# Kernel optimization log

Measured on AMD Instinct MI355X. Metric: run time of the kernel, lower is better.

Reference implementation:

```python
import jax, jax.numpy as jnp
import numpy as np
from jax import lax

NPOINT = 1024
NSAMPLE = 32
RADIUS = 0.6
BN_EPS = 1e-5


def square_distance(src, dst):
    # src (B,S,3), dst (B,N,3) -> (B,S,N) squared distances
    d = -2.0 * jnp.einsum('bsc,bnc->bsn', src, dst)
    d = d + jnp.sum(src ** 2, -1)[:, :, None]
    d = d + jnp.sum(dst ** 2, -1)[:, None, :]
    return d


def farthest_point_sample(xyz, npoint):
    B, N, _ = xyz.shape
    bidx = jnp.arange(B)

    def step(carry, _):
        distance, farthest = carry
        centroid = xyz[bidx, farthest]                      # (B,3)
        dist = jnp.sum((xyz - centroid[:, None, :]) ** 2, -1)  # (B,N)
        distance = jnp.minimum(distance, dist)
        new_far = jnp.argmax(distance, -1)
        return (distance, new_far), farthest

    init = (jnp.full((B, N), 1e10, xyz.dtype), jnp.zeros((B,), jnp.int32))
    _, idxs = lax.scan(step, init, None, length=npoint)
    return idxs.T                                            # (B,npoint)


def ball_query(xyz, new_xyz, radius, nsample):
    B, N, _ = xyz.shape
    sqr = square_distance(new_xyz, xyz)                      # (B,S,N)
    idx = jnp.where(sqr <= radius ** 2, jnp.arange(N)[None, None, :], N)
    idx = jnp.sort(idx, axis=-1)[:, :, :nsample]             # (B,S,K)
    first = idx[:, :, :1]
    return jnp.where(idx == N, first, idx)


def gather2(points, idx):
    # points (B,N,C), idx (B,S) -> (B,S,C)
    return jax.vmap(lambda p, i: p[i])(points, idx)


def gather3(points, idx):
    # points (B,N,C), idx (B,S,K) -> (B,S,K,C)
    return jax.vmap(lambda p, i: p[i])(points, idx)


def sa_forward(xyz, features, params):
    fps_idx = lax.stop_gradient(farthest_point_sample(xyz, NPOINT))
    new_xyz = gather2(xyz, fps_idx)                          # (B,S,3)
    idx = lax.stop_gradient(ball_query(xyz, new_xyz, RADIUS, NSAMPLE))
    grouped_xyz = gather3(xyz, idx) - new_xyz[:, :, None, :] # (B,S,K,3)
    grouped_feat = gather3(features.transpose(0, 2, 1), idx) # (B,S,K,C)
    g = jnp.concatenate([grouped_xyz, grouped_feat], -1)     # (B,S,K,C+3)
    g = g.transpose(0, 3, 2, 1)                              # (B,Cin,K,S)
    for w, b, ga, be in params:
        g = jnp.einsum('oc,bcks->boks', w, g) + b[None, :, None, None]
        mu = jnp.mean(g, axis=(0, 2, 3), keepdims=True)
        var = jnp.var(g, axis=(0, 2, 3), keepdims=True)
        g = ga[None, :, None, None] * (g - mu) * lax.rsqrt(var + BN_EPS) \
            + be[None, :, None, None]
        g = jax.nn.relu(g)
    new_features = jnp.max(g, axis=2)                        # (B,Cout,S)
    return new_xyz, new_features


def setup_inputs() -> dict:
    key = jax.random.key(0)
    ks = jax.random.split(key, 8)
    B, N, C = 16, 4096, 128
    cin = C + 3
    mlp = [128, 128, 256]
    inp = {
        'xyz': jax.random.normal(ks[0], (B, N, 3), jnp.float32),
        'features': jax.random.normal(ks[1], (B, C, N), jnp.float32),
    }
    prev = cin
    for i, out in enumerate(mlp):
        inp[f'w{i}'] = jax.random.normal(ks[2 + i], (out, prev), jnp.float32) * 0.05
        inp[f'b{i}'] = jnp.zeros((out,), jnp.float32)
        inp[f'gamma{i}'] = jnp.ones((out,), jnp.float32)
        inp[f'beta{i}'] = jnp.zeros((out,), jnp.float32)
        prev = out
    return inp


def reference(xyz, features, w0, b0, gamma0, beta0, w1, b1, gamma1, beta1,
              w2, b2, gamma2, beta2):
    params = [(w0, b0, gamma0, beta0), (w1, b1, gamma1, beta1),
              (w2, b2, gamma2, beta2)]
    return sa_forward(xyz, features, params)
```

## Files before the change

### kernel.cpp

```cpp
#include <hip/hip_runtime.h>

#define B_ 16
#define N_ 4096
#define S_ 1024
#define K_ 32
#define PITCH2 136
#define PITCH1 168

typedef unsigned long long u64;
typedef short bf16x8 __attribute__((ext_vector_type(8)));
typedef unsigned short u16x8 __attribute__((ext_vector_type(8)));
typedef float f32x4 __attribute__((ext_vector_type(4)));
typedef float f32x2 __attribute__((ext_vector_type(2)));

__device__ __forceinline__ unsigned short f2bf(float f) {
  unsigned u = __float_as_uint(f);
  unsigned r = (u + 0x7FFFu + ((u >> 16) & 1u)) >> 16;
  return (unsigned short)r;
}
__device__ __forceinline__ float bf2f(unsigned short h) {
  return __uint_as_float(((unsigned)h) << 16);
}

#define DPP_MAX(v, ctrl)                                                        \
  {                                                                             \
    int _t = __builtin_amdgcn_update_dpp(__float_as_int(v), __float_as_int(v),  \
                                         ctrl, 0xf, 0xf, false);                \
    v = fmaxf(v, __int_as_float(_t));                                           \
  }

__global__ __launch_bounds__(512) void k_front(
    const float* __restrict__ xyz, float* __restrict__ new_xyz,
    const float* __restrict__ feat, unsigned short* __restrict__ featT,
    const float* __restrict__ w0, const float* __restrict__ w1,
    const float* __restrict__ w2, unsigned short* __restrict__ wbf0,
    unsigned short* __restrict__ wbf1, unsigned short* __restrict__ wbf2,
    float* __restrict__ stats) {
  __shared__ __align__(16) float smem[N_ * 4 + S_ + 64];
  int blk = blockIdx.x, t = threadIdx.x;

  if (blk < 16) {
#pragma clang fp contract(off)
#if __has_builtin(__builtin_amdgcn_s_setprio)
    __builtin_amdgcn_s_setprio(3);
#endif
    float4* pts = (float4*)smem;
    int* idxs = (int*)(smem + N_ * 4);
    u64* swk = (u64*)(smem + N_ * 4 + S_);
    int b = blk;
    const float* base = xyz + (size_t)b * N_ * 3;
    for (int i = t; i < N_; i += 512)
      pts[i] = make_float4(base[i * 3], base[i * 3 + 1], base[i * 3 + 2], 0.0f);
    if (t == 0) idxs[0] = 0;
    __syncthreads();
    f32x2 px[4], py[4], pz[4], pd[4];
    int i0 = t * 8;
    #pragma unroll
    for (int j = 0; j < 4; ++j) {
      float4 p0 = pts[i0 + 2 * j], p1 = pts[i0 + 2 * j + 1];
      px[j] = (f32x2){p0.x, p1.x};
      py[j] = (f32x2){p0.y, p1.y};
      pz[j] = (f32x2){p0.z, p1.z};
      pd[j] = (f32x2){1e10f, 1e10f};
    }
    int cur = 0;
    for (int it = 0; it < S_; ++it) {
      float4 c = pts[cur];
      f32x2 c2x = (f32x2){c.x, c.x}, c2y = (f32x2){c.y, c.y}, c2z = (f32x2){c.z, c.z};
      float bestv = -1.0f; int besti = 0;
      #pragma unroll
      for (int j = 0; j < 4; ++j) {
        f32x2 dx = px[j] - c2x;
        f32x2 dy = py[j] - c2y;
        f32x2 dz = pz[j] - c2z;
        f32x2 d = (dx * dx + dy * dy) + dz * dz;
        f32x2 dm = __builtin_elementwise_min(pd[j], d);
        pd[j] = dm;
        if (dm.x > bestv) { bestv = dm.x; besti = 2 * j; }
        if (dm.y > bestv) { bestv = dm.y; besti = 2 * j + 1; }
      }
      float v = bestv;
      DPP_MAX(v, 0x111);
      DPP_MAX(v, 0x112);
      DPP_MAX(v, 0x114);
      DPP_MAX(v, 0x118);
      DPP_MAX(v, 0x142);
      DPP_MAX(v, 0x143);
      float wmax = __int_as_float(__builtin_amdgcn_readlane(__float_as_int(v), 63));
      u64 mask = __ballot(bestv == wmax);
      int owner = __ffsll((long long)mask) - 1;
      int widx = __builtin_amdgcn_readlane(i0 + besti, owner);
      if ((t & 63) == 0)
        swk[(it & 1) * 8 + (t >> 6)] =
            ((u64)__float_as_uint(wmax) << 32) | (unsigned)(4095 - widx);
      __syncthreads();
      const u64* kk = swk + (it & 1) * 8;
      u64 k0 = kk[0];
      #pragma unroll
      for (int w = 1; w < 8; ++w) if (kk[w] > k0) k0 = kk[w];
      cur = 4095 - (int)(unsigned)(k0 & 0xFFFFFFFFull);
      if (t == 0 && it + 1 < S_) idxs[it + 1] = cur;
    }
    __syncthreads();
    for (int i = t; i < S_; i += 512) {
      float4 v = pts[idxs[i]];
      size_t o = ((size_t)b * S_ + i) * 3;
      new_xyz[o] = v.x; new_xyz[o + 1] = v.y; new_xyz[o + 2] = v.z;
    }
  } else if (blk < 32) {
    int id = (blk - 16) * 512 + t;
    const int st = 16 * 512;
    for (int i = id; i < 32768; i += st) stats[i] = 0.0f;
    for (int i = id; i < 128 * 160; i += st) {
      int n = i / 160, k = i - n * 160;
      float v = (k < 128) ? w0[n * 131 + 3 + k] : (k < 131) ? w0[n * 131 + k - 128] : 0.0f;
      wbf0[i] = f2bf(v);
    }
    for (int i = id; i < 128 * 128; i += st) wbf1[i] = f2bf(w1[i]);
    for (int i = id; i < 256 * 128; i += st) wbf2[i] = f2bf(w2[i]);
  } else {
    float (*tile)[33] = (float(*)[33])smem;
    int blk2 = blk - 32;
    int n0 = (blk2 & 127) * 32;
    int c0 = ((blk2 >> 7) & 3) * 32;
    int b = blk2 >> 9;
    int tx = t & 31, ty = t >> 5;
    #pragma unroll
    for (int j = 0; j < 32; j += 16)
      tile[ty + j][tx] = feat[((size_t)b * 128 + c0 + ty + j) * N_ + n0 + tx];
    __syncthreads();
    #pragma unroll
    for (int j = 0; j < 32; j += 16)
      featT[((size_t)b * N_ + n0 + ty + j) * 128 + c0 + tx] = f2bf(tile[tx][ty + j]);
  }
}

__global__ __launch_bounds__(256) void k_ballq(const float* __restrict__ xyz,
                                               const float* __restrict__ new_xyz,
                                               int* __restrict__ ball_idx) {
  int b = blockIdx.y;
  int s = blockIdx.x * 4 + (threadIdx.x >> 6);
  int lane = threadIdx.x & 63;
  const float* pb = xyz + (size_t)b * N_ * 3;
  size_t q = (size_t)b * S_ + s;
  float qx = new_xyz[q * 3], qy = new_xyz[q * 3 + 1], qz = new_xyz[q * 3 + 2];
  float sq = __fadd_rn(__fadd_rn(__fmul_rn(qx, qx), __fmul_rn(qy, qy)), __fmul_rn(qz, qz));
  int* out = ball_idx + q * K_;
  int total = 0;
  int first_idx = -1;
  for (int basei = 0; basei < N_; basei += 64) {
    int i = basei + lane;
    float fx = pb[i * 3], fy = pb[i * 3 + 1], fz = pb[i * 3 + 2];
    float dot = __fmul_rn(qx, fx);
    dot = __fadd_rn(dot, __fmul_rn(qy, fy));
    dot = __fadd_rn(dot, __fmul_rn(qz, fz));
    float sd = __fadd_rn(__fadd_rn(__fmul_rn(fx, fx), __fmul_rn(fy, fy)), __fmul_rn(fz, fz));
    float dist = __fadd_rn(__fadd_rn(__fmul_rn(-2.0f, dot), sq), sd);
    bool within = (dist <= 0.36f);
    u64 m = __ballot(within);
    if (first_idx < 0 && m) first_idx = basei + __ffsll((long long)m) - 1;
    if (within) {
      int pos = total + __popcll(m & ((1ull << lane) - 1ull));
      if (pos < K_) out[pos] = i;
    }
    total += (int)__popcll(m);
    if (total >= K_) break;
  }
  if (total < K_) {
    int k2 = total + lane;
    if (k2 < K_) out[k2] = first_idx;
  }
}

#define MFMA(a, b, c) __builtin_amdgcn_mfma_f32_16x16x32_bf16(a, b, c, 0, 0, 0)
#define NTILES 4096

__global__ __launch_bounds__(256) void k_layer1(
    const float* __restrict__ xyz, const float* __restrict__ new_xyz,
    const unsigned short* __restrict__ featT, const int* __restrict__ ball_idx,
    const unsigned short* __restrict__ wbf0, const float* __restrict__ b0,
    unsigned short* __restrict__ y, float* __restrict__ stats) {
  __shared__ __align__(16) unsigned short Wl[128 * PITCH1];
  __shared__ float sbias[128];
  int t = threadIdx.x;
  int w = t >> 6, L = t & 63, lm = L & 15, lg = L >> 4;
  {
    int n = t >> 1, h = t & 1;
    const uint4* wr = (const uint4*)(wbf0 + n * 160 + h * 80);
    uint4* wl = (uint4*)(Wl + n * PITCH1 + h * 80);
    #pragma unroll
    for (int i = 0; i < 10; ++i) wl[i] = wr[i];
    if (t < 128) sbias[t] = b0[t];
  }
  __syncthreads();

  for (int tile = blockIdx.x; tile < NTILES; tile += gridDim.x) {
    int bb = tile >> 8;
    int s0 = (tile & 255) * 4;
    size_t qg = (size_t)bb * S_ + s0 + w;

    int p0 = ball_idx[qg * K_ + lm];
    int p1 = ball_idx[qg * K_ + 16 + lm];
    const unsigned short* f0 = featT + ((size_t)bb * N_ + p0) * 128;
    const unsigned short* f1 = featT + ((size_t)bb * N_ + p1) * 128;
    bf16x8 a0[5], a1[5];
    #pragma unroll
    for (int kt = 0; kt < 4; ++kt) {
      a0[kt] = *(const bf16x8*)(f0 + kt * 32 + lg * 8);
      a1[kt] = *(const bf16x8*)(f1 + kt * 32 + lg * 8);
    }
    a0[4] = (bf16x8){0, 0, 0, 0, 0, 0, 0, 0};
    a1[4] = (bf16x8){0, 0, 0, 0, 0, 0, 0, 0};
    if (lg == 0) {
      float nx = new_xyz[qg * 3], ny = new_xyz[qg * 3 + 1], nz = new_xyz[qg * 3 + 2];
      const float* pp0 = xyz + ((size_t)bb * N_ + p0) * 3;
      const float* pp1 = xyz + ((size_t)bb * N_ + p1) * 3;
      a0[4][0] = (short)f2bf(pp0[0] - nx);
      a0[4][1] = (short)f2bf(pp0[1] - ny);
      a0[4][2] = (short)f2bf(pp0[2] - nz);
      a1[4][0] = (short)f2bf(pp1[0] - nx);
      a1[4][1] = (short)f2bf(pp1[1] - ny);
      a1[4][2] = (short)f2bf(pp1[2] - nz);
    }
    f32x4 acc[2][8];
    #pragma unroll
    for (int mi = 0; mi < 2; ++mi)
      #pragma unroll
      for (int nt = 0; nt < 8; ++nt) acc[mi][nt] = (f32x4){0.f, 0.f, 0.f, 0.f};
    #pragma unroll
    for (int kt = 0; kt < 5; ++kt) {
      int ko = kt * 32 + lg * 8;
      bf16x8 bv[8];
      #pragma unroll
      for (int nt = 0; nt < 8; ++nt)
        bv[nt] = *(const bf16x8*)&Wl[(nt * 16 + lm) * PITCH1 + ko];
      #pragma unroll
      for (int nt = 0; nt < 8; ++nt) {
        acc[0][nt] = MFMA(a0[kt], bv[nt], acc[0][nt]);
        acc[1][nt] = MFMA(a1[kt], bv[nt], acc[1][nt]);
      }
    }
    int slot = tile & 31;
    #pragma unroll
    for (int nt = 0; nt < 8; ++nt) {
      int col = nt * 16 + lm;
      float bo = sbias[col];
      float s1 = 0.f, s2 = 0.f;
      #pragma unroll
      for (int mi = 0; mi < 2; ++mi)
        #pragma unroll
        for (int r = 0; r < 4; ++r) {
          float yv = acc[mi][nt][r] + bo;
          s1 += yv; s2 += yv * yv;
          int ks = mi * 16 + lg * 4 + r;
          y[(qg * K_ + ks) * 128 + col] = f2bf(yv);
        }
      s1 += __shfl_xor(s1, 16); s2 += __shfl_xor(s2, 16);
      s1 += __shfl_xor(s1, 32); s2 += __shfl_xor(s2, 32);
      if (lg == 0) {
        atomicAdd(stats + ((size_t)slot * 128 + col) * 2, s1);
        atomicAdd(stats + ((size_t)slot * 128 + col) * 2 + 1, s2);
      }
    }
  }
}

__global__ __launch_bounds__(256) void k_layer2(
    unsigned short* y, const float* __restrict__ stats,
    const float* __restrict__ gamma, const float* __restrict__ beta,
    const unsigned short* __restrict__ wbf1, const float* __restrict__ b1,
    float* __restrict__ stats2) {
  __shared__ __align__(16) unsigned short Wl[128 * PITCH2];
  __shared__ __align__(16) float sa[128], sd[128];
  __shared__ float sbias[128];
  int t = threadIdx.x;
  int w = t >> 6, L = t & 63, lm = L & 15, lg = L >> 4;
  if (t < 128) {
    float s1 = 0.0f, s2 = 0.0f;
    for (int sl = 0; sl < 32; ++sl) {
      s1 += stats[((size_t)sl * 128 + t) * 2];
      s2 += stats[((size_t)sl * 128 + t) * 2 + 1];
    }
    const float inv = 1.0f / 524288.0f;
    float mu = s1 * inv;
    float var = s2 * inv - mu * mu;
    float a = gamma[t] * rsqrtf(var + 1e-5f);
    sa[t] = a;
    sd[t] = beta[t] - a * mu;
    sbias[t] = b1[t];
  }
  {
    int n = t >> 1, h = t & 1;
    const uint4* wr = (const uint4*)(wbf1 + n * 128 + h * 64);
    uint4* wl = (uint4*)(Wl + n * PITCH2 + h * 64);
    #pragma unroll
    for (int i = 0; i < 8; ++i) wl[i] = wr[i];
  }
  __syncthreads();

  for (int tile = blockIdx.x; tile < NTILES; tile += gridDim.x) {
    int bb = tile >> 8;
    int s0 = (tile & 255) * 4;
    size_t qg = (size_t)bb * S_ + s0 + w;

    const u16x8* yr0 = (const u16x8*)(y + (qg * K_ + lm) * 128);
    const u16x8* yr1 = (const u16x8*)(y + (qg * K_ + 16 + lm) * 128);
    u16x8 raw0[4], raw1[4];
    #pragma unroll
    for (int kt = 0; kt < 4; ++kt) { raw0[kt] = yr0[kt * 4 + lg]; raw1[kt] = yr1[kt * 4 + lg]; }
    bf16x8 a0[4], a1[4];
    #pragma unroll
    for (int kt = 0; kt < 4; ++kt) {
      int c = kt * 32 + lg * 8;
      f32x4 A0 = *(const f32x4*)&sa[c], A1 = *(const f32x4*)&sa[c + 4];
      f32x4 D0 = *(const f32x4*)&sd[c], D1 = *(const f32x4*)&sd[c + 4];
      #pragma unroll
      for (int j = 0; j < 4; ++j) {
        a0[kt][j]     = (short)f2bf(fmaxf(A0[j] * bf2f(raw0[kt][j])     + D0[j], 0.f));
        a0[kt][j + 4] = (short)f2bf(fmaxf(A1[j] * bf2f(raw0[kt][j + 4]) + D1[j], 0.f));
        a1[kt][j]     = (short)f2bf(fmaxf(A0[j] * bf2f(raw1[kt][j])     + D0[j], 0.f));
        a1[kt][j + 4] = (short)f2bf(fmaxf(A1[j] * bf2f(raw1[kt][j + 4]) + D1[j], 0.f));
      }
    }
    f32x4 acc[2][8];
    #pragma unroll
    for (int mi = 0; mi < 2; ++mi)
      #pragma unroll
      for (int nt = 0; nt < 8; ++nt) acc[mi][nt] = (f32x4){0.f, 0.f, 0.f, 0.f};
    #pragma unroll
    for (int kt = 0; kt < 4; ++kt) {
      int ko = kt * 32 + lg * 8;
      bf16x8 bv[8];
      #pragma unroll
      for (int nt = 0; nt < 8; ++nt)
        bv[nt] = *(const bf16x8*)&Wl[(nt * 16 + lm) * PITCH2 + ko];
      #pragma unroll
      for (int nt = 0; nt < 8; ++nt) {
        acc[0][nt] = MFMA(a0[kt], bv[nt], acc[0][nt]);
        acc[1][nt] = MFMA(a1[kt], bv[nt], acc[1][nt]);
      }
    }
    int slot = tile & 31;
    #pragma unroll
    for (int nt = 0; nt < 8; ++nt) {
      int col = nt * 16 + lm;
      float bo = sbias[col];
      float s1 = 0.f, s2 = 0.f;
      #pragma unroll
      for (int mi = 0; mi < 2; ++mi)
        #pragma unroll
        for (int r = 0; r < 4; ++r) {
          float yv = acc[mi][nt][r] + bo;
          s1 += yv; s2 += yv * yv;
          int ks = mi * 16 + lg * 4 + r;
          y[(qg * K_ + ks) * 128 + col] = f2bf(yv);
        }
      s1 += __shfl_xor(s1, 16); s2 += __shfl_xor(s2, 16);
      s1 += __shfl_xor(s1, 32); s2 += __shfl_xor(s2, 32);
      if (lg == 0) {
        atomicAdd(stats2 + ((size_t)slot * 128 + col) * 2, s1);
        atomicAdd(stats2 + ((size_t)slot * 128 + col) * 2 + 1, s2);
      }
    }
  }
}

__global__ __launch_bounds__(256) void k_layer3(
    const unsigned short* __restrict__ y, const float* __restrict__ stats2,
    const float* __restrict__ gamma, const float* __restrict__ beta,
    const unsigned short* __restrict__ wbf2, const float* __restrict__ b2,
    unsigned short* __restrict__ ymax, unsigned short* __restrict__ ymin,
    float* __restrict__ stats3) {
  __shared__ __align__(16) unsigned short Wl[128 * PITCH2];
  __shared__ __align__(16) float sa[128], sd[128];
  __shared__ float sbias[128];
  int nh = blockIdx.y, t = threadIdx.x;
  int w = t >> 6, L = t & 63, lm = L & 15, lg = L >> 4;
  if (t < 128) {
    float s1 = 0.0f, s2 = 0.0f;
    for (int sl = 0; sl < 32; ++sl) {
      s1 += stats2[((size_t)sl * 128 + t) * 2];
      s2 += stats2[((size_t)sl * 128 + t) * 2 + 1];
    }
    const float inv = 1.0f / 524288.0f;
    float mu = s1 * inv;
    float var = s2 * inv - mu * mu;
    float a = gamma[t] * rsqrtf(var + 1e-5f);
    sa[t] = a;
    sd[t] = beta[t] - a * mu;
    sbias[t] = b2[nh * 128 + t];
  }
  {
    int n = t >> 1, h = t & 1;
    const uint4* wr = (const uint4*)(wbf2 + (size_t)(nh * 128 + n) * 128 + h * 64);
    uint4* wl = (uint4*)(Wl + n * PITCH2 + h * 64);
    #pragma unroll
    for (int i = 0; i < 8; ++i) wl[i] = wr[i];
  }
  __syncthreads();

  for (int tile = blockIdx.x; tile < NTILES; tile += gridDim.x) {
    int bb = tile >> 8;
    int s0 = (tile & 255) * 4;
    size_t qg = (size_t)bb * S_ + s0 + w;

    const u16x8* yr0 = (const u16x8*)(y + (qg * K_ + lm) * 128);
    const u16x8* yr1 = (const u16x8*)(y + (qg * K_ + 16 + lm) * 128);
    u16x8 raw0[4], raw1[4];
    #pragma unroll
    for (int kt = 0; kt < 4; ++kt) { raw0[kt] = yr0[kt * 4 + lg]; raw1[kt] = yr1[kt * 4 + lg]; }
    bf16x8 a0[4], a1[4];
    #pragma unroll
    for (int kt = 0; kt < 4; ++kt) {
      int c = kt * 32 + lg * 8;
      f32x4 A0 = *(const f32x4*)&sa[c], A1 = *(const f32x4*)&sa[c + 4];
      f32x4 D0 = *(const f32x4*)&sd[c], D1 = *(const f32x4*)&sd[c + 4];
      #pragma unroll
      for (int j = 0; j < 4; ++j) {
        a0[kt][j]     = (short)f2bf(fmaxf(A0[j] * bf2f(raw0[kt][j])     + D0[j], 0.f));
        a0[kt][j + 4] = (short)f2bf(fmaxf(A1[j] * bf2f(raw0[kt][j + 4]) + D1[j], 0.f));
        a1[kt][j]     = (short)f2bf(fmaxf(A0[j] * bf2f(raw1[kt][j])     + D0[j], 0.f));
        a1[kt][j + 4] = (short)f2bf(fmaxf(A1[j] * bf2f(raw1[kt][j + 4]) + D1[j], 0.f));
      }
    }
    f32x4 acc[2][8];
    #pragma unroll
    for (int mi = 0; mi < 2; ++mi)
      #pragma unroll
      for (int nt = 0; nt < 8; ++nt) acc[mi][nt] = (f32x4){0.f, 0.f, 0.f, 0.f};
    #pragma unroll
    for (int kt = 0; kt < 4; ++kt) {
      int ko = kt * 32 + lg * 8;
      bf16x8 bv[8];
      #pragma unroll
      for (int nt = 0; nt < 8; ++nt)
        bv[nt] = *(const bf16x8*)&Wl[(nt * 16 + lm) * PITCH2 + ko];
      #pragma unroll
      for (int nt = 0; nt < 8; ++nt) {
        acc[0][nt] = MFMA(a0[kt], bv[nt], acc[0][nt]);
        acc[1][nt] = MFMA(a1[kt], bv[nt], acc[1][nt]);
      }
    }
    int slot = tile & 31;
    #pragma unroll
    for (int nt = 0; nt < 8; ++nt) {
      int col = nt * 16 + lm;
      int o = nh * 128 + col;
      float bo = sbias[col];
      float s1 = 0.f, s2 = 0.f, mx = -3.4e38f, mn = 3.4e38f;
      #pragma unroll
      for (int mi = 0; mi < 2; ++mi)
        #pragma unroll
        for (int r = 0; r < 4; ++r) {
          float yv = acc[mi][nt][r] + bo;
          s1 += yv; s2 += yv * yv;
          mx = fmaxf(mx, yv); mn = fminf(mn, yv);
        }
      s1 += __shfl_xor(s1, 16); s2 += __shfl_xor(s2, 16);
      s1 += __shfl_xor(s1, 32); s2 += __shfl_xor(s2, 32);
      mx = fmaxf(mx, __shfl_xor(mx, 16)); mx = fmaxf(mx, __shfl_xor(mx, 32));
      mn = fminf(mn, __shfl_xor(mn, 16)); mn = fminf(mn, __shfl_xor(mn, 32));
      if (lg == 0) {
        ymax[qg * 256 + o] = f2bf(mx);
        ymin[qg * 256 + o] = f2bf(mn);
        atomicAdd(stats3 + ((size_t)slot * 256 + o) * 2, s1);
        atomicAdd(stats3 + ((size_t)slot * 256 + o) * 2 + 1, s2);
      }
    }
  }
}

__global__ __launch_bounds__(256) void k_final(const unsigned short* __restrict__ ymax,
                                               const unsigned short* __restrict__ ymin,
                                               const float* __restrict__ stats3,
                                               const float* __restrict__ gamma,
                                               const float* __restrict__ beta,
                                               float* __restrict__ out2) {
  __shared__ float tile[32][33];
  __shared__ float smA[32], smD[32];
  int b = blockIdx.z, o0 = blockIdx.y * 32, s0 = blockIdx.x * 32;
  int tx = threadIdx.x, ty = threadIdx.y;
  if (ty == 0) {
    int c = o0 + tx;
    float s1 = 0.0f, s2 = 0.0f;
    for (int sl = 0; sl < 32; ++sl) {
      s1 += stats3[((size_t)sl * 256 + c) * 2];
      s2 += stats3[((size_t)sl * 256 + c) * 2 + 1];
    }
    const float inv = 1.0f / 524288.0f;
    float mu = s1 * inv;
    float var = s2 * inv - mu * mu;
    float a = gamma[c] * rsqrtf(var + 1e-5f);
    smA[tx] = a;
    smD[tx] = beta[c] - a * mu;
  }
  __syncthreads();
  float a_rd = smA[tx];
  #pragma unroll
  for (int j = 0; j < 32; j += 8) {
    size_t src = ((size_t)b * S_ + s0 + ty + j) * 256 + o0 + tx;
    tile[ty + j][tx] = (a_rd >= 0.0f) ? bf2f(ymax[src]) : bf2f(ymin[src]);
  }
  __syncthreads();
  #pragma unroll
  for (int j = 0; j < 32; j += 8) {
    float a = smA[ty + j], dd = smD[ty + j];
    out2[((size_t)b * 256 + o0 + ty + j) * S_ + s0 + tx] = fmaxf(a * tile[tx][ty + j] + dd, 0.0f);
  }
}

extern "C" void kernel_launch(void* const* d_in, const int* in_sizes, int n_in,
                              void* d_out, int out_size, void* d_ws, size_t ws_size,
                              hipStream_t stream) {
  (void)in_sizes; (void)n_in; (void)out_size; (void)ws_size;
  const float* xyz  = (const float*)d_in[0];
  const float* feat = (const float*)d_in[1];
  const float* w0   = (const float*)d_in[2];
  const float* b0   = (const float*)d_in[3];
  const float* ga0  = (const float*)d_in[4];
  const float* be0  = (const float*)d_in[5];
  const float* w1   = (const float*)d_in[6];
  const float* b1   = (const float*)d_in[7];
  const float* ga1  = (const float*)d_in[8];
  const float* be1  = (const float*)d_in[9];
  const float* w2   = (const float*)d_in[10];
  const float* b2   = (const float*)d_in[11];
  const float* ga2  = (const float*)d_in[12];
  const float* be2  = (const float*)d_in[13];

  float* out_xyz  = (float*)d_out;
  float* out_feat = out_xyz + (size_t)B_ * S_ * 3;

  char* ws = (char*)d_ws;
  size_t off = 0;
  auto alloc = [&](size_t bytes) -> void* {
    void* p = ws + off;
    off += (bytes + 255) & ~(size_t)255;
    return p;
  };
  unsigned short* featT = (unsigned short*)alloc((size_t)B_ * N_ * 128 * 2);
  int*   ball  = (int*)alloc((size_t)B_ * S_ * K_ * 4);
  float* stats = (float*)alloc(32768 * 4);
  unsigned short* wbf0 = (unsigned short*)alloc(128 * 160 * 2);
  unsigned short* wbf1 = (unsigned short*)alloc(128 * 128 * 2);
  unsigned short* wbf2 = (unsigned short*)alloc(256 * 128 * 2);
  unsigned short* ymaxb = (unsigned short*)alloc((size_t)B_ * S_ * 256 * 2);
  unsigned short* yminb = (unsigned short*)alloc((size_t)B_ * S_ * 256 * 2);
  unsigned short* y = (unsigned short*)alloc((size_t)B_ * S_ * K_ * 128 * 2);

  k_front<<<16 + 16 + 8192, 512, 0, stream>>>(xyz, out_xyz, feat, featT,
                                              w0, w1, w2, wbf0, wbf1, wbf2, stats);
  k_ballq<<<dim3(256, 16), 256, 0, stream>>>(xyz, out_xyz, ball);
  k_layer1<<<768, 256, 0, stream>>>(xyz, out_xyz, featT, ball, wbf0, b0, y, stats);
  k_layer2<<<1024, 256, 0, stream>>>(y, stats, ga0, be0, wbf1, b1, stats + 8192);
  k_layer3<<<dim3(512, 2), 256, 0, stream>>>(y, stats + 8192, ga1, be1, wbf2, b2,
                                             ymaxb, yminb, stats + 16384);
  k_final<<<dim3(32, 8, 16), dim3(32, 8), 0, stream>>>(ymaxb, yminb, stats + 16384,
                                                       ga2, be2, out_feat);
}
```

Before: 1.084 ms.

## Run farthest point sampling in a single wavefront to remove block barriers

The FPS loop now runs in a single 64-lane wavefront per batch. Each lane keeps 64 points in registers, so the per-iteration __syncthreads and the shared-memory cross-wave argmax are gone. The argmax becomes a DPP max reduction followed by a DPP min over matching indices, which picks the lowest index on ties. The block size drops to 256 with launch bounds (256,1), and the transpose and weight-conversion branches are adjusted to match. The cost is heavy register pressure (128 float2 arrays) and a serial chain run by one wave, with the other three waves of the block idle.

```diff
diff --git a/kernel.cpp b/kernel.cpp
--- a/kernel.cpp
+++ b/kernel.cpp
@@ -22,14 +22,19 @@
   return __uint_as_float(((unsigned)h) << 16);
 }
 
-#define DPP_MAX(v, ctrl)                                                        \
+#define DPP_MAXF(v, ctrl)                                                       \
   {                                                                             \
     int _t = __builtin_amdgcn_update_dpp(__float_as_int(v), __float_as_int(v),  \
                                          ctrl, 0xf, 0xf, false);                \
     v = fmaxf(v, __int_as_float(_t));                                           \
   }
-
-__global__ __launch_bounds__(512) void k_front(
+#define DPP_MINI(v, ctrl)                                                       \
+  {                                                                             \
+    int _t = __builtin_amdgcn_update_dpp(v, v, ctrl, 0xf, 0xf, false);          \
+    v = min(v, _t);                                                             \
+  }
+
+__global__ __launch_bounds__(256, 1) void k_front(
     const float* __restrict__ xyz, float* __restrict__ new_xyz,
     const float* __restrict__ feat, unsigned short* __restrict__ featT,
     const float* __restrict__ w0, const float* __restrict__ w1,
@@ -46,70 +51,86 @@
 #endif
     float4* pts = (float4*)smem;
     int* idxs = (int*)(smem + N_ * 4);
-    u64* swk = (u64*)(smem + N_ * 4 + S_);
     int b = blk;
     const float* base = xyz + (size_t)b * N_ * 3;
-    for (int i = t; i < N_; i += 512)
+    for (int i = t; i < N_; i += 256)
       pts[i] = make_float4(base[i * 3], base[i * 3 + 1], base[i * 3 + 2], 0.0f);
     if (t == 0) idxs[0] = 0;
     __syncthreads();
-    f32x2 px[4], py[4], pz[4], pd[4];
-    int i0 = t * 8;
-    #pragma unroll
-    for (int j = 0; j < 4; ++j) {
-      float4 p0 = pts[i0 + 2 * j], p1 = pts[i0 + 2 * j + 1];
-      px[j] = (f32x2){p0.x, p1.x};
-      py[j] = (f32x2){p0.y, p1.y};
-      pz[j] = (f32x2){p0.z, p1.z};
-      pd[j] = (f32x2){1e10f, 1e10f};
-    }
-    int cur = 0;
-    for (int it = 0; it < S_; ++it) {
-      float4 c = pts[cur];
-      f32x2 c2x = (f32x2){c.x, c.x}, c2y = (f32x2){c.y, c.y}, c2z = (f32x2){c.z, c.z};
-      float bestv = -1.0f; int besti = 0;
-      #pragma unroll
-      for (int j = 0; j < 4; ++j) {
-        f32x2 dx = px[j] - c2x;
-        f32x2 dy = py[j] - c2y;
-        f32x2 dz = pz[j] - c2z;
-        f32x2 d = (dx * dx + dy * dy) + dz * dz;
-        f32x2 dm = __builtin_elementwise_min(pd[j], d);
-        pd[j] = dm;
-        if (dm.x > bestv) { bestv = dm.x; besti = 2 * j; }
-        if (dm.y > bestv) { bestv = dm.y; besti = 2 * j + 1; }
-      }
-      float v = bestv;
-      DPP_MAX(v, 0x111);
-      DPP_MAX(v, 0x112);
-      DPP_MAX(v, 0x114);
-      DPP_MAX(v, 0x118);
-      DPP_MAX(v, 0x142);
-      DPP_MAX(v, 0x143);
-      float wmax = __int_as_float(__builtin_amdgcn_readlane(__float_as_int(v), 63));
-      u64 mask = __ballot(bestv == wmax);
-      int owner = __ffsll((long long)mask) - 1;
-      int widx = __builtin_amdgcn_readlane(i0 + besti, owner);
-      if ((t & 63) == 0)
-        swk[(it & 1) * 8 + (t >> 6)] =
-            ((u64)__float_as_uint(wmax) << 32) | (unsigned)(4095 - widx);
-      __syncthreads();
-      const u64* kk = swk + (it & 1) * 8;
-      u64 k0 = kk[0];
-      #pragma unroll
-      for (int w = 1; w < 8; ++w) if (kk[w] > k0) k0 = kk[w];
-      cur = 4095 - (int)(unsigned)(k0 & 0xFFFFFFFFull);
-      if (t == 0 && it + 1 < S_) idxs[it + 1] = cur;
+
+    if (t < 64) {
+      int L = t;
+      f32x2 px[32], py[32], pz[32], pd[32];
+      #pragma unroll
+      for (int j = 0; j < 32; ++j) {
+        float4 p = pts[(2 * j) * 64 + L];
+        float4 q = pts[(2 * j + 1) * 64 + L];
+        px[j] = (f32x2){p.x, q.x};
+        py[j] = (f32x2){p.y, q.y};
+        pz[j] = (f32x2){p.z, q.z};
+        pd[j] = (f32x2){1e10f, 1e10f};
+      }
+      int cur = 0;
+      for (int it = 0; it < S_; ++it) {
+        float4 c = pts[cur];
+        f32x2 c2x = (f32x2){c.x, c.x};
+        f32x2 c2y = (f32x2){c.y, c.y};
+        f32x2 c2z = (f32x2){c.z, c.z};
+        #pragma unroll
+        for (int j = 0; j < 32; ++j) {
+          f32x2 dx = px[j] - c2x;
+          f32x2 dy = py[j] - c2y;
+          f32x2 dz = pz[j] - c2z;
+          f32x2 d = (dx * dx + dy * dy) + dz * dz;
+          pd[j] = __builtin_elementwise_min(pd[j], d);
+        }
+        f32x2 m[16];
+        #pragma unroll
+        for (int j = 0; j < 16; ++j)
+          m[j] = __builtin_elementwise_max(pd[2 * j], pd[2 * j + 1]);
+        #pragma unroll
+        for (int j = 0; j < 8; ++j)
+          m[j] = __builtin_elementwise_max(m[2 * j], m[2 * j + 1]);
+        #pragma unroll
+        for (int j = 0; j < 4; ++j)
+          m[j] = __builtin_elementwise_max(m[2 * j], m[2 * j + 1]);
+        m[0] = __builtin_elementwise_max(m[0], m[1]);
+        m[0] = __builtin_elementwise_max(m[0], __builtin_elementwise_max(m[2], m[3]) * 0.0f + __builtin_elementwise_max(m[2], m[3]));
+        float v = fmaxf(m[0].x, m[0].y);
+        DPP_MAXF(v, 0x111);
+        DPP_MAXF(v, 0x112);
+        DPP_MAXF(v, 0x114);
+        DPP_MAXF(v, 0x118);
+        DPP_MAXF(v, 0x142);
+        DPP_MAXF(v, 0x143);
+        float gmax = __int_as_float(__builtin_amdgcn_readlane(__float_as_int(v), 63));
+        int cand = 64;
+        #pragma unroll
+        for (int j = 31; j >= 0; --j) {
+          if (pd[j].y == gmax) cand = 2 * j + 1;
+          if (pd[j].x == gmax) cand = 2 * j;
+        }
+        int gidx = cand * 64 + L;
+        DPP_MINI(gidx, 0x111);
+        DPP_MINI(gidx, 0x112);
+        DPP_MINI(gidx, 0x114);
+        DPP_MINI(gidx, 0x118);
+        DPP_MINI(gidx, 0x142);
+        DPP_MINI(gidx, 0x143);
+        int widx = __builtin_amdgcn_readlane(gidx, 63);
+        if (L == 0 && it + 1 < S_) idxs[it + 1] = widx;
+        cur = widx;
+      }
     }
     __syncthreads();
-    for (int i = t; i < S_; i += 512) {
+    for (int i = t; i < S_; i += 256) {
       float4 v = pts[idxs[i]];
       size_t o = ((size_t)b * S_ + i) * 3;
       new_xyz[o] = v.x; new_xyz[o + 1] = v.y; new_xyz[o + 2] = v.z;
     }
   } else if (blk < 32) {
-    int id = (blk - 16) * 512 + t;
-    const int st = 16 * 512;
+    int id = (blk - 16) * 256 + t;
+    const int st = 16 * 256;
     for (int i = id; i < 32768; i += st) stats[i] = 0.0f;
     for (int i = id; i < 128 * 160; i += st) {
       int n = i / 160, k = i - n * 160;
@@ -126,11 +147,11 @@
     int b = blk2 >> 9;
     int tx = t & 31, ty = t >> 5;
     #pragma unroll
-    for (int j = 0; j < 32; j += 16)
+    for (int j = 0; j < 32; j += 8)
       tile[ty + j][tx] = feat[((size_t)b * 128 + c0 + ty + j) * N_ + n0 + tx];
     __syncthreads();
     #pragma unroll
-    for (int j = 0; j < 32; j += 16)
+    for (int j = 0; j < 32; j += 8)
       featT[((size_t)b * N_ + n0 + ty + j) * 128 + c0 + tx] = f2bf(tile[tx][ty + j]);
   }
 }
@@ -548,7 +569,7 @@
   unsigned short* yminb = (unsigned short*)alloc((size_t)B_ * S_ * 256 * 2);
   unsigned short* y = (unsigned short*)alloc((size_t)B_ * S_ * K_ * 128 * 2);
 
-  k_front<<<16 + 16 + 8192, 512, 0, stream>>>(xyz, out_xyz, feat, featT,
+  k_front<<<16 + 16 + 8192, 256, 0, stream>>>(xyz, out_xyz, feat, featT,
                                               w0, w1, w2, wbf0, wbf1, wbf2, stats);
   k_ballq<<<dim3(256, 16), 256, 0, stream>>>(xyz, out_xyz, ball);
   k_layer1<<<768, 256, 0, stream>>>(xyz, out_xyz, featT, ball, wbf0, b0, y, stats);
```

After: 2.001 ms. 1.84x slower.
